# Performance work log

Measured on AMD Instinct MI355X. Metric: run time of the kernel, lower is better.

## Reference

```python
import jax, jax.numpy as jnp
import numpy as np

NEG_SLOPE = 0.2
EPS = 1e-16


def gatv2_conv(x, src, dst, n_nodes, Wl, Wr, att, bias):
    """GATv2Conv, heads=1, add_self_loops handled by caller via src/dst.
    x: [N, Fin]; src/dst: [E] (message j->i means src=j, dst=i).
    Wl, Wr: [Fin, Fout]; att: [Fout]; bias: [Fout].
    """
    xl = x @ Wl  # [N, Fout] (source transform)
    xr = x @ Wr  # [N, Fout] (target transform)
    # per-edge attention logit: a^T LeakyReLU(xl[j] + xr[i])
    h = xl[src] + xr[dst]                      # [E, Fout]
    e = jax.nn.leaky_relu(h, NEG_SLOPE) @ att  # [E]
    # segment softmax over incoming edges of each dst node
    m = jax.ops.segment_max(e, dst, num_segments=n_nodes)   # [N]
    ex = jnp.exp(e - m[dst])                                 # [E]
    denom = jax.ops.segment_sum(ex, dst, num_segments=n_nodes)  # [N]
    alpha = ex / (denom[dst] + EPS)                          # [E]
    # scatter-aggregate weighted source messages
    out = jax.ops.segment_sum(alpha[:, None] * xl[src], dst, num_segments=n_nodes)
    return out + bias


def glorot(key, shape):
    lim = np.sqrt(6.0 / (shape[0] + shape[1]))
    return jax.random.uniform(key, shape, jnp.float32, -lim, lim)


def setup_inputs() -> dict:
    key = jax.random.key(0)
    ks = jax.random.split(key, 9)
    N, E, Fin, H, Fout = 50000, 800000, 128, 64, 2
    x = jax.random.normal(ks[0], (N, Fin), jnp.float32)
    edge_index = jax.random.randint(ks[1], (2, E), 0, N, jnp.int64)
    return {
        "x": x,
        "edge_index": edge_index,
        "Wl1": glorot(ks[2], (Fin, H)),
        "Wr1": glorot(ks[3], (Fin, H)),
        "att1": glorot(ks[4], (H, 1))[:, 0],
        "b1": jnp.zeros((H,), jnp.float32),
        "Wl2": glorot(ks[5], (H, Fout)),
        "Wr2": glorot(ks[6], (H, Fout)),
        "att2": glorot(ks[7], (Fout, 1))[:, 0],
        "b2": jnp.zeros((Fout,), jnp.float32),
    }


def reference(x, edge_index, Wl1, Wr1, att1, b1, Wl2, Wr2, att2, b2):
    n_nodes = x.shape[0]
    # PyG GATv2Conv adds self-loops by default
    loops = jnp.arange(n_nodes, dtype=edge_index.dtype)
    src = jnp.concatenate([edge_index[0], loops])
    dst = jnp.concatenate([edge_index[1], loops])
    # eval mode: dropout is identity; the initial relu/dropout result is dead code
    h = gatv2_conv(x, src, dst, n_nodes, Wl1, Wr1, att1, b1)
    out = gatv2_conv(h, src, dst, n_nodes, Wl2, Wr2, att2, b2)
    return out
```

## Files before the change

### kernel.cpp

```cpp
#include <hip/hip_runtime.h>
#include <math.h>

#define FIN 128
#define H 64
#define FOUT 2
#define NEG_SLOPE 0.2f
#define EPS 1e-16f

#define SCAN_CHUNK 2048

typedef __attribute__((ext_vector_type(8))) short s8v;
typedef __attribute__((ext_vector_type(4))) float f4v;

__device__ __forceinline__ void load_bs(const int* __restrict__ blocksum, int nscan,
                                        int* bs, int tid){
  if(tid < 64){
    int v = (tid < nscan)? blocksum[tid] : 0;
    int incl = v;
    #pragma unroll
    for(int o=1;o<64;o<<=1){ int u=__shfl_up(incl,o); if(tid>=o) incl+=u; }
    bs[tid] = incl - v;
  }
  __syncthreads();
}

__global__ void k_prep(int* __restrict__ deg, int N, int ZB,
                       const float* __restrict__ Wl, const float* __restrict__ Wr,
                       unsigned short* __restrict__ pWh, unsigned short* __restrict__ pWe){
  int b = blockIdx.x;
  if(b < ZB){
    int i = b*256 + threadIdx.x;
    if(i < N) deg[i] = 0;
    return;
  }
  int idx = (b - ZB)*256 + threadIdx.x;
  int lane = idx & 63;
  int ctk  = idx >> 6;
  int k0   = (ctk & 3) * 32;
  int ct   = ctk >> 2;
  int c    = ct*16 + (lane & 15);
  int kb   = k0 + (lane >> 4)*8;
  const float* Wp = (c < 64) ? (Wl + c) : (Wr + (c - 64));
  #pragma unroll
  for(int j=0;j<8;j++){
    float v = Wp[(size_t)(kb + j)*H];
    unsigned u = __float_as_uint(v);
    unsigned short hb = (unsigned short)(u >> 16);
    float hv = __uint_as_float(((unsigned)hb) << 16);
    float ev = v - hv;
    unsigned short eb = (unsigned short)(__float_as_uint(ev) >> 16);
    pWh[(size_t)idx*8 + j] = hb;
    pWe[(size_t)idx*8 + j] = eb;
  }
}

__global__ __launch_bounds__(256) void k_gemm_mfma(
    const float* __restrict__ x,
    const unsigned short* __restrict__ pWh, const unsigned short* __restrict__ pWe,
    float* __restrict__ xl, float* __restrict__ xr,
    unsigned short* __restrict__ xlb, int N){
  int tid = threadIdx.x;
  int lane = tid & 63, wid = tid >> 6;
  int rowbase = blockIdx.x*64 + wid*16;
  int r = lane & 15, g = lane >> 4;

  int arow = rowbase + r; if(arow > N-1) arow = N-1;
  const float* xrow = x + (size_t)arow*FIN;

  s8v ah[4], ae[4];
  #pragma unroll
  for(int k0=0;k0<4;k0++){
    float4 va = *(const float4*)(xrow + k0*32 + g*8);
    float4 vb = *(const float4*)(xrow + k0*32 + g*8 + 4);
    float xs_[8] = {va.x,va.y,va.z,va.w,vb.x,vb.y,vb.z,vb.w};
    #pragma unroll
    for(int j=0;j<8;j++){
      unsigned u = __float_as_uint(xs_[j]);
      unsigned short hb = (unsigned short)(u >> 16);
      ah[k0][j] = (short)hb;
      float ev = xs_[j] - __uint_as_float(((unsigned)hb) << 16);
      ae[k0][j] = (short)(unsigned short)(__float_as_uint(ev) >> 16);
    }
  }

  #pragma unroll 2
  for(int ct=0;ct<8;ct++){
    f4v a = (f4v){0.f,0.f,0.f,0.f};
    #pragma unroll
    for(int k0=0;k0<4;k0++){
      size_t boff = ((size_t)(ct*4 + k0)*64 + lane)*8;
      s8v bh = *(const s8v*)(pWh + boff);
      s8v be = *(const s8v*)(pWe + boff);
      a = __builtin_amdgcn_mfma_f32_16x16x32_bf16(ah[k0], bh, a, 0,0,0);
      a = __builtin_amdgcn_mfma_f32_16x16x32_bf16(ah[k0], be, a, 0,0,0);
      a = __builtin_amdgcn_mfma_f32_16x16x32_bf16(ae[k0], bh, a, 0,0,0);
    }
    float* dst = (ct < 4) ? xl : xr;
    int cc = (ct & 3)*16 + r;
    #pragma unroll
    for(int rr=0;rr<4;rr++){
      int row = rowbase + g*4 + rr;
      if(row < N){
        dst[(size_t)row*H + cc] = a[rr];
        if(ct < 4){
          unsigned u = __float_as_uint(a[rr]);
          xlb[(size_t)row*H + cc] = (unsigned short)((u + 0x7FFF + ((u>>16)&1)) >> 16);
        }
      }
    }
  }
}

__global__ void k_degree(const int* __restrict__ ei, int E, int Etot,
                         int* __restrict__ deg, int* __restrict__ rank){
  int i0 = (blockIdx.x*blockDim.x + threadIdx.x)*4;
  if(i0 >= Etot) return;
  if(i0 + 4 <= E && (E & 3) == 0){
    int4 d4 = *(const int4*)(ei + E + i0);
    int r0 = atomicAdd(&deg[d4.x],1);
    int r1 = atomicAdd(&deg[d4.y],1);
    int r2 = atomicAdd(&deg[d4.z],1);
    int r3 = atomicAdd(&deg[d4.w],1);
    *(int4*)(rank + i0) = make_int4(r0,r1,r2,r3);
  } else if(i0 >= E && i0 + 4 <= Etot){
    int v = i0 - E;
    int r0 = atomicAdd(&deg[v+0],1);
    int r1 = atomicAdd(&deg[v+1],1);
    int r2 = atomicAdd(&deg[v+2],1);
    int r3 = atomicAdd(&deg[v+3],1);
    *(int4*)(rank + i0) = make_int4(r0,r1,r2,r3);
  } else {
    #pragma unroll
    for(int q=0;q<4;q++){
      int i = i0+q; if(i>=Etot) break;
      int dst = (i<E) ? ei[E+i] : (i-E);
      rank[i] = atomicAdd(&deg[dst],1);
    }
  }
}

__global__ __launch_bounds__(256) void k_scan_a(const int* __restrict__ deg, int n,
                                                int* __restrict__ rowptr,
                                                int* __restrict__ blocksum){
  __shared__ int wsum[4];
  int tid = threadIdx.x, lane = tid & 63, wid = tid >> 6;
  int idx = blockIdx.x*SCAN_CHUNK + tid*8;
  int v[8];
  if(idx + 8 <= n){
    int4 a = *(const int4*)(deg + idx);
    int4 b = *(const int4*)(deg + idx + 4);
    v[0]=a.x;v[1]=a.y;v[2]=a.z;v[3]=a.w;v[4]=b.x;v[5]=b.y;v[6]=b.z;v[7]=b.w;
  } else {
    #pragma unroll
    for(int i=0;i<8;i++) v[i] = (idx+i<n)? deg[idx+i] : 0;
  }
  int pre[8]; int st=0;
  #pragma unroll
  for(int i=0;i<8;i++){ pre[i]=st; st+=v[i]; }
  int incl = st;
  #pragma unroll
  for(int o=1;o<64;o<<=1){ int u=__shfl_up(incl,o); if(lane>=o) incl+=u; }
  if(lane==63) wsum[wid]=incl;
  __syncthreads();
  if(tid==0){ int accu=0; for(int i=0;i<4;i++){ int t=wsum[i]; wsum[i]=accu; accu+=t; } }
  __syncthreads();
  int toff = wsum[wid] + incl - st;
  if(idx + 8 <= n){
    int4 o0 = make_int4(toff+pre[0],toff+pre[1],toff+pre[2],toff+pre[3]);
    int4 o1 = make_int4(toff+pre[4],toff+pre[5],toff+pre[6],toff+pre[7]);
    *(int4*)(rowptr+idx)=o0; *(int4*)(rowptr+idx+4)=o1;
  } else {
    #pragma unroll
    for(int i=0;i<8;i++) if(idx+i<n) rowptr[idx+i]=toff+pre[i];
  }
  if(tid==255){
    blocksum[blockIdx.x] = toff + st;
    if(blockIdx.x == gridDim.x-1) rowptr[n] = toff + st;
  }
}

__global__ void k_fill(const int* __restrict__ ei, int E, int Etot,
                       const int* __restrict__ rowptr,
                       const int* __restrict__ blocksum, int nscan,
                       const int* __restrict__ rank, int* __restrict__ csr_src){
  __shared__ int bs[64];
  int tid = threadIdx.x;
  load_bs(blocksum, nscan, bs, tid);
  int i0 = (blockIdx.x*blockDim.x + tid)*4;
  if(i0 >= Etot) return;
  if(i0 + 4 <= E && (E & 3) == 0){
    int4 s4 = *(const int4*)(ei + i0);
    int4 d4 = *(const int4*)(ei + E + i0);
    int4 r4 = *(const int4*)(rank + i0);
    csr_src[rowptr[d4.x] + bs[d4.x>>11] + r4.x] = s4.x;
    csr_src[rowptr[d4.y] + bs[d4.y>>11] + r4.y] = s4.y;
    csr_src[rowptr[d4.z] + bs[d4.z>>11] + r4.z] = s4.z;
    csr_src[rowptr[d4.w] + bs[d4.w>>11] + r4.w] = s4.w;
  } else if(i0 >= E && i0 + 4 <= Etot){
    int4 r4 = *(const int4*)(rank + i0);
    int v = i0 - E;
    csr_src[rowptr[v+0] + bs[(v+0)>>11] + r4.x] = v+0;
    csr_src[rowptr[v+1] + bs[(v+1)>>11] + r4.y] = v+1;
    csr_src[rowptr[v+2] + bs[(v+2)>>11] + r4.z] = v+2;
    csr_src[rowptr[v+3] + bs[(v+3)>>11] + r4.w] = v+3;
  } else {
    #pragma unroll
    for(int q=0;q<4;q++){
      int i = i0+q; if(i>=Etot) break;
      int src, dst;
      if(i<E){ src = ei[i]; dst = ei[E+i]; } else { src = i-E; dst = i-E; }
      csr_src[rowptr[dst] + bs[dst>>11] + rank[i]] = src;
    }
  }
}

__global__ void k_node1f(const int* __restrict__ rowptr, const int* __restrict__ blocksum,
                         int nscan, const int* __restrict__ csr_src,
                         const unsigned short* __restrict__ xlb, const float* __restrict__ xr,
                         const float* __restrict__ att, const float* __restrict__ b1,
                         const float* __restrict__ Wl2, const float* __restrict__ Wr2,
                         float* __restrict__ xl2, float* __restrict__ xr2, int N){
  __shared__ int bs[64];
  int tid = threadIdx.x;
  load_bs(blocksum, nscan, bs, tid);
  int node = blockIdx.x*16 + (tid>>4);
  int gl = tid & 15;
  if(node >= N) return;
  int f4 = gl*4;
  float4 attv = *(const float4*)(att + f4);
  float4 xrv  = *(const float4*)(xr + (size_t)node*H + f4);
  int s = rowptr[node]   + bs[node>>11];
  int t = rowptr[node+1] + bs[(node+1)>>11];
  float d = 0.f;
  float ax=0.f, ay=0.f, az=0.f, aw=0.f;

  for(int k=s; k<t; k+=8){
    int tl = t - 1;
    int ks[8]; float4 xv[8]; float msk[8];
    #pragma unroll
    for(int j=0;j<8;j++){
      int kj = k + j;
      ks[j] = (kj < t) ? kj : tl;
      msk[j] = (kj < t) ? 1.f : 0.f;
    }
    int ss[8];
    #pragma unroll
    for(int j=0;j<8;j++) ss[j] = csr_src[ks[j]];
    #pragma unroll
    for(int j=0;j<8;j++){
      ushort4 uv = *(const ushort4*)(xlb + (size_t)ss[j]*H + f4);
      xv[j].x = __uint_as_float((unsigned)uv.x << 16);
      xv[j].y = __uint_as_float((unsigned)uv.y << 16);
      xv[j].z = __uint_as_float((unsigned)uv.z << 16);
      xv[j].w = __uint_as_float((unsigned)uv.w << 16);
    }
    #pragma unroll
    for(int j=0;j<8;j++){
      float h0 = xv[j].x + xrv.x, h1 = xv[j].y + xrv.y;
      float h2 = xv[j].z + xrv.z, h3 = xv[j].w + xrv.w;
      float l0 = (h0>0.f)? h0 : NEG_SLOPE*h0;
      float l1 = (h1>0.f)? h1 : NEG_SLOPE*h1;
      float l2 = (h2>0.f)? h2 : NEG_SLOPE*h2;
      float l3 = (h3>0.f)? h3 : NEG_SLOPE*h3;
      float e = l0*attv.x + l1*attv.y + l2*attv.z + l3*attv.w;
      #pragma unroll
      for(int o=1;o<16;o<<=1) e += __shfl_xor(e,o);
      float w = msk[j] * __expf(e);
      d  += w;
      ax += w*xv[j].x; ay += w*xv[j].y; az += w*xv[j].z; aw += w*xv[j].w;
    }
  }

  float inv = 1.f/(d + EPS);
  float4 bv = *(const float4*)(b1 + f4);
  float h0 = ax*inv + bv.x, h1 = ay*inv + bv.y;
  float h2 = az*inv + bv.z, h3 = aw*inv + bv.w;
  float p0 = h0*Wl2[(f4+0)*FOUT+0] + h1*Wl2[(f4+1)*FOUT+0] + h2*Wl2[(f4+2)*FOUT+0] + h3*Wl2[(f4+3)*FOUT+0];
  float p1 = h0*Wl2[(f4+0)*FOUT+1] + h1*Wl2[(f4+1)*FOUT+1] + h2*Wl2[(f4+2)*FOUT+1] + h3*Wl2[(f4+3)*FOUT+1];
  float p2 = h0*Wr2[(f4+0)*FOUT+0] + h1*Wr2[(f4+1)*FOUT+0] + h2*Wr2[(f4+2)*FOUT+0] + h3*Wr2[(f4+3)*FOUT+0];
  float p3 = h0*Wr2[(f4+0)*FOUT+1] + h1*Wr2[(f4+1)*FOUT+1] + h2*Wr2[(f4+2)*FOUT+1] + h3*Wr2[(f4+3)*FOUT+1];
  #pragma unroll
  for(int o=1;o<16;o<<=1){
    p0 += __shfl_xor(p0,o); p1 += __shfl_xor(p1,o);
    p2 += __shfl_xor(p2,o); p3 += __shfl_xor(p3,o);
  }
  if(gl==0){
    *(float2*)(xl2 + node*2) = make_float2(p0,p1);
    *(float2*)(xr2 + node*2) = make_float2(p2,p3);
  }
}

__global__ void k_node2(const int* __restrict__ rowptr, const int* __restrict__ blocksum,
                        int nscan, const int* __restrict__ csr_src,
                        const float* __restrict__ xl2, const float* __restrict__ xr2,
                        const float* __restrict__ att2, const float* __restrict__ b2,
                        float* __restrict__ out, int N){
  __shared__ int bs[64];
  int tid = threadIdx.x;
  load_bs(blocksum, nscan, bs, tid);
  int node = blockIdx.x*16 + (tid>>4);
  int gl = tid & 15;
  if(node >= N) return;
  int s = rowptr[node]   + bs[node>>11];
  int t = rowptr[node+1] + bs[(node+1)>>11];
  float2 xrv = *(const float2*)(xr2 + node*2);
  float a0 = att2[0], a1 = att2[1];
  float den=0.f, n0=0.f, n1=0.f;
  for(int k=s+gl; k<t; k+=16){
    int src = csr_src[k];
    float2 xs = *(const float2*)(xl2 + src*2);
    float h0 = xs.x + xrv.x, h1 = xs.y + xrv.y;
    float l0 = (h0>0.f)? h0 : NEG_SLOPE*h0;
    float l1 = (h1>0.f)? h1 : NEG_SLOPE*h1;
    float ex = __expf(l0*a0 + l1*a1);
    den += ex; n0 += ex*xs.x; n1 += ex*xs.y;
  }
  #pragma unroll
  for(int o=1;o<16;o<<=1){
    den += __shfl_xor(den,o);
    n0  += __shfl_xor(n0,o);
    n1  += __shfl_xor(n1,o);
  }
  if(gl==0){
    float inv = 1.f/(den + EPS);
    out[node*2+0] = n0*inv + b2[0];
    out[node*2+1] = n1*inv + b2[1];
  }
}

extern "C" void kernel_launch(void* const* d_in, const int* in_sizes, int n_in,
                              void* d_out, int out_size, void* d_ws, size_t ws_size,
                              hipStream_t stream){
  const float* x    = (const float*)d_in[0];
  const int*   ei   = (const int*)d_in[1];
  const float* Wl1  = (const float*)d_in[2];
  const float* Wr1  = (const float*)d_in[3];
  const float* att1 = (const float*)d_in[4];
  const float* b1   = (const float*)d_in[5];
  const float* Wl2  = (const float*)d_in[6];
  const float* Wr2  = (const float*)d_in[7];
  const float* att2 = (const float*)d_in[8];
  const float* b2   = (const float*)d_in[9];
  int N = in_sizes[0]/FIN;
  int E = in_sizes[1]/2;
  int Etot = E + N;
  int nscan = (N + SCAN_CHUNK - 1) / SCAN_CHUNK;
  int nquad = (Etot + 3) / 4;
  int ZB = (N + 255) / 256;

  char* w = (char*)d_ws;
  size_t off = 0;
  auto alloc = [&](size_t bytes)->void*{
    void* p = w + off;
    off = (off + bytes + 255) & ~(size_t)255;
    return p;
  };
  float* xl1     = (float*)alloc((size_t)N*H*4);
  float* xr1     = (float*)alloc((size_t)N*H*4);
  unsigned short* xlb = (unsigned short*)alloc((size_t)N*H*2);
  int*   csr_src = (int*)  alloc((size_t)Etot*4);
  int*   rank    = (int*)  alloc((size_t)Etot*4);
  int*   deg     = (int*)  alloc((size_t)N*4);
  int*   rowptr  = (int*)  alloc((size_t)(N+1)*4);
  int*   blocksum= (int*)  alloc((size_t)64*4);
  float* xl2     = (float*)alloc((size_t)N*2*4);
  float* xr2     = (float*)alloc((size_t)N*2*4);
  unsigned short* pWh = (unsigned short*)alloc((size_t)2048*8*2);
  unsigned short* pWe = (unsigned short*)alloc((size_t)2048*8*2);

  k_prep<<<ZB+8, 256, 0, stream>>>(deg, N, ZB, Wl1, Wr1, pWh, pWe);
  k_gemm_mfma<<<(N+63)/64, 256, 0, stream>>>(x, pWh, pWe, xl1, xr1, xlb, N);
  k_degree<<<(nquad+255)/256,256,0,stream>>>(ei, E, Etot, deg, rank);
  k_scan_a<<<nscan,256,0,stream>>>(deg, N, rowptr, blocksum);
  k_fill<<<(nquad+255)/256,256,0,stream>>>(ei, E, Etot, rowptr, blocksum, nscan, rank, csr_src);
  k_node1f<<<(N+15)/16, 256, 0, stream>>>(rowptr, blocksum, nscan, csr_src,
                                          xlb, xr1, att1, b1, Wl2, Wr2, xl2, xr2, N);
  k_node2<<<(N+15)/16, 256, 0, stream>>>(rowptr, blocksum, nscan, csr_src,
                                         xl2, xr2, att2, b2, (float*)d_out, N);
}
```

Measured before the change: 123.6 us.

## Fuse degree counting into GEMM launch and split node1 edges across two half-groups

Merges the degree/rank atomic pass into the MFMA GEMM kernel as extra blocks, so the two independent stages run in one launch and can overlap. The degree and fill kernels now handle 8 edges per thread instead of 4. The first-layer aggregation kernel assigns 32 lanes per node, with two 16-lane halves taking alternating 8-edge chunks, then combines the halves by shuffle and splits the left/right layer-2 projections between them. This is meant to shorten per-node serial edge loops and cut launch overhead, at the cost of more shuffles and less work per lane on low-degree nodes.

New measurement: 122.1 us. No clear change (-1.2%).

```diff
diff --git a/kernel.cpp b/kernel.cpp
--- a/kernel.cpp
+++ b/kernel.cpp
@@ -54,12 +54,53 @@
   }
 }
 
-__global__ __launch_bounds__(256) void k_gemm_mfma(
+__global__ __launch_bounds__(256) void k_gemm_deg(
     const float* __restrict__ x,
     const unsigned short* __restrict__ pWh, const unsigned short* __restrict__ pWe,
     float* __restrict__ xl, float* __restrict__ xr,
-    unsigned short* __restrict__ xlb, int N){
+    unsigned short* __restrict__ xlb, int N, int GG,
+    const int* __restrict__ ei, int E, int Etot,
+    int* __restrict__ deg, int* __restrict__ rank){
   int tid = threadIdx.x;
+  if((int)blockIdx.x >= GG){
+    int i0 = (((int)blockIdx.x - GG)*256 + tid)*8;
+    if(i0 >= Etot) return;
+    if(i0 + 8 <= E && (E & 3) == 0){
+      int4 da = *(const int4*)(ei + E + i0);
+      int4 db = *(const int4*)(ei + E + i0 + 4);
+      int r0 = atomicAdd(&deg[da.x],1);
+      int r1 = atomicAdd(&deg[da.y],1);
+      int r2 = atomicAdd(&deg[da.z],1);
+      int r3 = atomicAdd(&deg[da.w],1);
+      int r4 = atomicAdd(&deg[db.x],1);
+      int r5 = atomicAdd(&deg[db.y],1);
+      int r6 = atomicAdd(&deg[db.z],1);
+      int r7 = atomicAdd(&deg[db.w],1);
+      *(int4*)(rank + i0)     = make_int4(r0,r1,r2,r3);
+      *(int4*)(rank + i0 + 4) = make_int4(r4,r5,r6,r7);
+    } else if(i0 >= E && i0 + 8 <= Etot){
+      int v = i0 - E;
+      int r0 = atomicAdd(&deg[v+0],1);
+      int r1 = atomicAdd(&deg[v+1],1);
+      int r2 = atomicAdd(&deg[v+2],1);
+      int r3 = atomicAdd(&deg[v+3],1);
+      int r4 = atomicAdd(&deg[v+4],1);
+      int r5 = atomicAdd(&deg[v+5],1);
+      int r6 = atomicAdd(&deg[v+6],1);
+      int r7 = atomicAdd(&deg[v+7],1);
+      *(int4*)(rank + i0)     = make_int4(r0,r1,r2,r3);
+      *(int4*)(rank + i0 + 4) = make_int4(r4,r5,r6,r7);
+    } else {
+      #pragma unroll
+      for(int q=0;q<8;q++){
+        int i = i0+q; if(i>=Etot) break;
+        int dst = (i<E) ? ei[E+i] : (i-E);
+        rank[i] = atomicAdd(&deg[dst],1);
+      }
+    }
+    return;
+  }
+
   int lane = tid & 63, wid = tid >> 6;
   int rowbase = blockIdx.x*64 + wid*16;
   int r = lane & 15, g = lane >> 4;
@@ -107,34 +148,6 @@
           xlb[(size_t)row*H + cc] = (unsigned short)((u + 0x7FFF + ((u>>16)&1)) >> 16);
         }
       }
-    }
-  }
-}
-
-__global__ void k_degree(const int* __restrict__ ei, int E, int Etot,
-                         int* __restrict__ deg, int* __restrict__ rank){
-  int i0 = (blockIdx.x*blockDim.x + threadIdx.x)*4;
-  if(i0 >= Etot) return;
-  if(i0 + 4 <= E && (E & 3) == 0){
-    int4 d4 = *(const int4*)(ei + E + i0);
-    int r0 = atomicAdd(&deg[d4.x],1);
-    int r1 = atomicAdd(&deg[d4.y],1);
-    int r2 = atomicAdd(&deg[d4.z],1);
-    int r3 = atomicAdd(&deg[d4.w],1);
-    *(int4*)(rank + i0) = make_int4(r0,r1,r2,r3);
-  } else if(i0 >= E && i0 + 4 <= Etot){
-    int v = i0 - E;
-    int r0 = atomicAdd(&deg[v+0],1);
-    int r1 = atomicAdd(&deg[v+1],1);
-    int r2 = atomicAdd(&deg[v+2],1);
-    int r3 = atomicAdd(&deg[v+3],1);
-    *(int4*)(rank + i0) = make_int4(r0,r1,r2,r3);
-  } else {
-    #pragma unroll
-    for(int q=0;q<4;q++){
-      int i = i0+q; if(i>=Etot) break;
-      int dst = (i<E) ? ei[E+i] : (i-E);
-      rank[i] = atomicAdd(&deg[dst],1);
     }
   }
 }
@@ -186,26 +199,38 @@
   __shared__ int bs[64];
   int tid = threadIdx.x;
   load_bs(blocksum, nscan, bs, tid);
-  int i0 = (blockIdx.x*blockDim.x + tid)*4;
+  int i0 = (blockIdx.x*blockDim.x + tid)*8;
   if(i0 >= Etot) return;
-  if(i0 + 4 <= E && (E & 3) == 0){
-    int4 s4 = *(const int4*)(ei + i0);
-    int4 d4 = *(const int4*)(ei + E + i0);
-    int4 r4 = *(const int4*)(rank + i0);
-    csr_src[rowptr[d4.x] + bs[d4.x>>11] + r4.x] = s4.x;
-    csr_src[rowptr[d4.y] + bs[d4.y>>11] + r4.y] = s4.y;
-    csr_src[rowptr[d4.z] + bs[d4.z>>11] + r4.z] = s4.z;
-    csr_src[rowptr[d4.w] + bs[d4.w>>11] + r4.w] = s4.w;
-  } else if(i0 >= E && i0 + 4 <= Etot){
-    int4 r4 = *(const int4*)(rank + i0);
+  if(i0 + 8 <= E && (E & 3) == 0){
+    int4 sa = *(const int4*)(ei + i0);
+    int4 sb = *(const int4*)(ei + i0 + 4);
+    int4 da = *(const int4*)(ei + E + i0);
+    int4 db = *(const int4*)(ei + E + i0 + 4);
+    int4 ra = *(const int4*)(rank + i0);
+    int4 rb = *(const int4*)(rank + i0 + 4);
+    csr_src[rowptr[da.x] + bs[da.x>>11] + ra.x] = sa.x;
+    csr_src[rowptr[da.y] + bs[da.y>>11] + ra.y] = sa.y;
+    csr_src[rowptr[da.z] + bs[da.z>>11] + ra.z] = sa.z;
+    csr_src[rowptr[da.w] + bs[da.w>>11] + ra.w] = sa.w;
+    csr_src[rowptr[db.x] + bs[db.x>>11] + rb.x] = sb.x;
+    csr_src[rowptr[db.y] + bs[db.y>>11] + rb.y] = sb.y;
+    csr_src[rowptr[db.z] + bs[db.z>>11] + rb.z] = sb.z;
+    csr_src[rowptr[db.w] + bs[db.w>>11] + rb.w] = sb.w;
+  } else if(i0 >= E && i0 + 8 <= Etot){
+    int4 ra = *(const int4*)(rank + i0);
+    int4 rb = *(const int4*)(rank + i0 + 4);
     int v = i0 - E;
-    csr_src[rowptr[v+0] + bs[(v+0)>>11] + r4.x] = v+0;
-    csr_src[rowptr[v+1] + bs[(v+1)>>11] + r4.y] = v+1;
-    csr_src[rowptr[v+2] + bs[(v+2)>>11] + r4.z] = v+2;
-    csr_src[rowptr[v+3] + bs[(v+3)>>11] + r4.w] = v+3;
+    csr_src[rowptr[v+0] + bs[(v+0)>>11] + ra.x] = v+0;
+    csr_src[rowptr[v+1] + bs[(v+1)>>11] + ra.y] = v+1;
+    csr_src[rowptr[v+2] + bs[(v+2)>>11] + ra.z] = v+2;
+    csr_src[rowptr[v+3] + bs[(v+3)>>11] + ra.w] = v+3;
+    csr_src[rowptr[v+4] + bs[(v+4)>>11] + rb.x] = v+4;
+    csr_src[rowptr[v+5] + bs[(v+5)>>11] + rb.y] = v+5;
+    csr_src[rowptr[v+6] + bs[(v+6)>>11] + rb.z] = v+6;
+    csr_src[rowptr[v+7] + bs[(v+7)>>11] + rb.w] = v+7;
   } else {
     #pragma unroll
-    for(int q=0;q<4;q++){
+    for(int q=0;q<8;q++){
       int i = i0+q; if(i>=Etot) break;
       int src, dst;
       if(i<E){ src = ei[i]; dst = ei[E+i]; } else { src = i-E; dst = i-E; }
@@ -223,7 +248,8 @@
   __shared__ int bs[64];
   int tid = threadIdx.x;
   load_bs(blocksum, nscan, bs, tid);
-  int node = blockIdx.x*16 + (tid>>4);
+  int node = blockIdx.x*8 + (tid>>5);
+  int half = (tid >> 4) & 1;
   int gl = tid & 15;
   if(node >= N) return;
   int f4 = gl*4;
@@ -234,7 +260,7 @@
   float d = 0.f;
   float ax=0.f, ay=0.f, az=0.f, aw=0.f;
 
-  for(int k=s; k<t; k+=8){
+  for(int k = s + half*8; k < t; k += 16){
     int tl = t - 1;
     int ks[8]; float4 xv[8]; float msk[8];
     #pragma unroll
@@ -271,22 +297,25 @@
     }
   }
 
+  d  += __shfl_xor(d,16);
+  ax += __shfl_xor(ax,16); ay += __shfl_xor(ay,16);
+  az += __shfl_xor(az,16); aw += __shfl_xor(aw,16);
+
   float inv = 1.f/(d + EPS);
   float4 bv = *(const float4*)(b1 + f4);
   float h0 = ax*inv + bv.x, h1 = ay*inv + bv.y;
   float h2 = az*inv + bv.z, h3 = aw*inv + bv.w;
-  float p0 = h0*Wl2[(f4+0)*FOUT+0] + h1*Wl2[(f4+1)*FOUT+0] + h2*Wl2[(f4+2)*FOUT+0] + h3*Wl2[(f4+3)*FOUT+0];
-  float p1 = h0*Wl2[(f4+0)*FOUT+1] + h1*Wl2[(f4+1)*FOUT+1] + h2*Wl2[(f4+2)*FOUT+1] + h3*Wl2[(f4+3)*FOUT+1];
-  float p2 = h0*Wr2[(f4+0)*FOUT+0] + h1*Wr2[(f4+1)*FOUT+0] + h2*Wr2[(f4+2)*FOUT+0] + h3*Wr2[(f4+3)*FOUT+0];
-  float p3 = h0*Wr2[(f4+0)*FOUT+1] + h1*Wr2[(f4+1)*FOUT+1] + h2*Wr2[(f4+2)*FOUT+1] + h3*Wr2[(f4+3)*FOUT+1];
+  const float* Wp = half ? Wr2 : Wl2;
+  float pa = h0*Wp[(f4+0)*FOUT+0] + h1*Wp[(f4+1)*FOUT+0] + h2*Wp[(f4+2)*FOUT+0] + h3*Wp[(f4+3)*FOUT+0];
+  float pb = h0*Wp[(f4+0)*FOUT+1] + h1*Wp[(f4+1)*FOUT+1] + h2*Wp[(f4+2)*FOUT+1] + h3*Wp[(f4+3)*FOUT+1];
   #pragma unroll
   for(int o=1;o<16;o<<=1){
-    p0 += __shfl_xor(p0,o); p1 += __shfl_xor(p1,o);
-    p2 += __shfl_xor(p2,o); p3 += __shfl_xor(p3,o);
+    pa += __shfl_xor(pa,o); pb += __shfl_xor(pb,o);
   }
   if(gl==0){
-    *(float2*)(xl2 + node*2) = make_float2(p0,p1);
-    *(float2*)(xr2 + node*2) = make_float2(p2,p3);
+    float2 pv = make_float2(pa,pb);
+    if(half==0) *(float2*)(xl2 + node*2) = pv;
+    else        *(float2*)(xr2 + node*2) = pv;
   }
 }
 
@@ -345,8 +374,10 @@
   int E = in_sizes[1]/2;
   int Etot = E + N;
   int nscan = (N + SCAN_CHUNK - 1) / SCAN_CHUNK;
-  int nquad = (Etot + 3) / 4;
+  int noct  = (Etot + 7) / 8;
   int ZB = (N + 255) / 256;
+  int GG = (N + 63) / 64;
+  int GDO = (noct + 255) / 256;
 
   char* w = (char*)d_ws;
   size_t off = 0;
@@ -369,12 +400,12 @@
   unsigned short* pWe = (unsigned short*)alloc((size_t)2048*8*2);
 
   k_prep<<<ZB+8, 256, 0, stream>>>(deg, N, ZB, Wl1, Wr1, pWh, pWe);
-  k_gemm_mfma<<<(N+63)/64, 256, 0, stream>>>(x, pWh, pWe, xl1, xr1, xlb, N);
-  k_degree<<<(nquad+255)/256,256,0,stream>>>(ei, E, Etot, deg, rank);
+  k_gemm_deg<<<GG+GDO, 256, 0, stream>>>(x, pWh, pWe, xl1, xr1, xlb, N, GG,
+                                         ei, E, Etot, deg, rank);
   k_scan_a<<<nscan,256,0,stream>>>(deg, N, rowptr, blocksum);
-  k_fill<<<(nquad+255)/256,256,0,stream>>>(ei, E, Etot, rowptr, blocksum, nscan, rank, csr_src);
-  k_node1f<<<(N+15)/16, 256, 0, stream>>>(rowptr, blocksum, nscan, csr_src,
-                                          xlb, xr1, att1, b1, Wl2, Wr2, xl2, xr2, N);
+  k_fill<<<GDO,256,0,stream>>>(ei, E, Etot, rowptr, blocksum, nscan, rank, csr_src);
+  k_node1f<<<(N+7)/8, 256, 0, stream>>>(rowptr, blocksum, nscan, csr_src,
+                                        xlb, xr1, att1, b1, Wl2, Wr2, xl2, xr2, N);
   k_node2<<<(N+15)/16, 256, 0, stream>>>(rowptr, blocksum, nscan, csr_src,
                                          xl2, xr2, att2, b2, (float*)d_out, N);
 }
```
